# Kernel tuning notes

Hardware: AMD Instinct MI355X
Metric: run time of the kernel (lower is better)

The kernel has to match this reference:

```python
import jax, jax.numpy as jnp
import numpy as np

N = 100000      # num_nodes
E = 1600000     # num_edges (avg degree 16)
EMB = 128       # emb_dim
HID = 128       # hidden_size
REPR = 64       # repr_dim


def setup_inputs() -> dict:
    key = jax.random.key(0)
    k0, k1, k2, k3 = jax.random.split(key, 4)
    edge_index = jax.random.randint(k0, (2, E), 0, N)
    node_emb = jax.random.normal(k1, (N, EMB), jnp.float32) * 0.1
    # GCNConv weights: glorot-like init, bias zeros (PyG default)
    W1 = jax.random.normal(k2, (EMB, HID), jnp.float32) * (1.0 / np.sqrt(EMB))
    b1 = jnp.zeros((HID,), jnp.float32)
    W2 = jax.random.normal(k3, (HID, REPR), jnp.float32) * (1.0 / np.sqrt(HID))
    b2 = jnp.zeros((REPR,), jnp.float32)
    return {"edge_index": edge_index, "node_emb": node_emb,
            "W1": W1, "b1": b1, "W2": W2, "b2": b2}


def reference(edge_index, node_emb, W1, b1, W2, b2):
    # PyG GCNConv: add self-loops, symmetric degree normalization,
    # out = scatter_add(norm * (x W)[src] -> dst) + b
    loops = jnp.arange(N, dtype=edge_index.dtype)
    src = jnp.concatenate([edge_index[0], loops])  # [E+N]
    dst = jnp.concatenate([edge_index[1], loops])
    deg = jax.ops.segment_sum(jnp.ones_like(src, dtype=node_emb.dtype), dst,
                              num_segments=N)
    dinv = jax.lax.rsqrt(deg)  # deg >= 1 thanks to self-loops
    norm = dinv[src] * dinv[dst]  # [E+N]

    def gcn_conv(x, W, b):
        h = x @ W                                   # [N, out]
        msg = norm[:, None] * h[src]                # gather + scale, [E+N, out]
        return jax.ops.segment_sum(msg, dst, num_segments=N) + b

    x = jax.nn.relu(gcn_conv(node_emb, W1, b1))
    # F.dropout(training=False) is identity in eval mode
    return gcn_conv(x, W2, b2)
```

## Files before the change

### kernel.cpp

```cpp
#include <hip/hip_runtime.h>
#include <hip/hip_bf16.h>
#include <stdint.h>


static constexpr int KD = 128;
static constexpr int BSH = 9;
static constexpr int MAXB = 256;
static constexpr int CHUNK = 8192;
static constexpr int CAP = 12288;

typedef short bf16x8 __attribute__((ext_vector_type(8)));
typedef float f32x4  __attribute__((ext_vector_type(4)));
typedef float f32x2  __attribute__((ext_vector_type(2)));

__device__ __forceinline__ unsigned short f2bf(float f) {
    __hip_bfloat16 b = __float2bfloat16(f);
    return *reinterpret_cast<unsigned short*>(&b);
}
__device__ __forceinline__ float bflo(unsigned v) { return __uint_as_float(v << 16); }
__device__ __forceinline__ float bfhi(unsigned v) { return __uint_as_float(v & 0xffff0000u); }
__device__ __forceinline__ unsigned pk2(float lo, float hi) {
    return (unsigned)f2bf(lo) | ((unsigned)f2bf(hi) << 16);
}
__device__ __forceinline__ void accp(f32x2* a, uint4 v) {
    f32x2 t;
    t.x = bflo(v.x); t.y = bfhi(v.x); a[0] += t;
    t.x = bflo(v.y); t.y = bfhi(v.y); a[1] += t;
    t.x = bflo(v.z); t.y = bfhi(v.z); a[2] += t;
    t.x = bflo(v.w); t.y = bfhi(v.w); a[3] += t;
}

__global__ __launch_bounds__(256) void init_misc(const float* __restrict__ W1,
        const float* __restrict__ W2, unsigned short* __restrict__ Wt1,
        unsigned short* __restrict__ Wt2, int* __restrict__ bcur, int nbuck) {
    int t = blockIdx.x * 256 + threadIdx.x;
    if (t < 128 * 128) {
        int k = t >> 7, nn = t & 127;
        Wt1[nn * 128 + k] = f2bf(W1[t]);
    } else if (t < 128 * 128 + 128 * 64) {
        int i = t - 128 * 128;
        int k = i >> 6, nn = i & 63;
        Wt2[nn * 128 + k] = f2bf(W2[i]);
    } else if (t < 128 * 128 + 128 * 64 + MAXB) {
        int b = t - (128 * 128 + 128 * 64);
        bcur[b] = b * CAP;
    }
}

__global__ __launch_bounds__(256) void multisplit(const int* __restrict__ src,
        const int* __restrict__ dst, int* __restrict__ bcur,
        int* __restrict__ packed, int e, int nbuck) {
    __shared__ int cnt[MAXB], lbase[MAXB], wbase[MAXB], vcnt[MAXB], scanbuf[256];
    __shared__ int buf[CHUNK];
    const int t = threadIdx.x;
    const int e0 = blockIdx.x * CHUNK;
    const int m = min(CHUNK, e - e0);

    for (int i = t; i < nbuck; i += 256) cnt[i] = 0;
    __syncthreads();
    for (int i = t; i < m; i += 256) atomicAdd(&cnt[dst[e0 + i] >> BSH], 1);
    __syncthreads();
    int v = (t < nbuck) ? cnt[t] : 0;
    scanbuf[t] = v;
    __syncthreads();
    for (int off = 1; off < 256; off <<= 1) {
        int u = (t >= off) ? scanbuf[t - off] : 0;
        __syncthreads();
        scanbuf[t] += u;
        __syncthreads();
    }
    int excl = scanbuf[t] - v;
    if (t < nbuck) {
        lbase[t] = excl;
        vcnt[t] = v;
        wbase[t] = v ? atomicAdd(&bcur[t], v) : 0;
        cnt[t] = excl;
    }
    __syncthreads();
    for (int i = t; i < m; i += 256) {
        int d = dst[e0 + i], s = src[e0 + i];
        int b = d >> BSH;
        int p = atomicAdd(&cnt[b], 1);
        buf[p] = ((d & ((1 << BSH) - 1)) << 22) | s;
    }
    __syncthreads();
    int wv = t >> 6, ln = t & 63;
    for (int b = wv; b < nbuck; b += 4) {
        int c = vcnt[b], st = lbase[b], g = wbase[b];
        int end = min(c, (b + 1) * CAP - g);
        for (int i = ln; i < end; i += 64) packed[g + i] = buf[st + i];
    }
}

__global__ __launch_bounds__(256) void bucket_build(const int* __restrict__ packed,
        const int* __restrict__ bcur, int* __restrict__ roff, int* __restrict__ degN,
        float* __restrict__ dinv, int* __restrict__ csr, int n) {
    __shared__ int deg[1 << BSH];
    __shared__ int cur[1 << BSH];
    __shared__ int wsum[4];
    const int t = threadIdx.x;
    const int b = blockIdx.x;
    const int nodeBase = b << BSH;
    const int nn = min(1 << BSH, n - nodeBase);
    const int e0 = b * CAP, e1 = bcur[b];

    for (int i = t; i < (1 << BSH); i += 256) deg[i] = 0;
    __syncthreads();
    for (int i = e0 + t; i < e1; i += 256)
        atomicAdd(&deg[(unsigned)packed[i] >> 22], 1);
    __syncthreads();

    const int i0 = t * 2;
    int d0 = deg[i0], d1 = deg[i0 + 1];
    int tsum = d0 + d1;
    int lane = t & 63, wv = t >> 6;
    int v = tsum;
    for (int off = 1; off < 64; off <<= 1) {
        int u = __shfl_up(v, off, 64);
        if (lane >= off) v += u;
    }
    if (lane == 63) wsum[wv] = v;
    __syncthreads();
    int woff = 0;
    for (int i = 0; i < wv; ++i) woff += wsum[i];
    int excl = v - tsum + woff;
    int p0 = excl, p1 = excl + d0;
    cur[i0] = p0; cur[i0 + 1] = p1;
    if (i0 < nn) {
        roff[nodeBase + i0] = e0 + p0;
        degN[nodeBase + i0] = d0;
        dinv[nodeBase + i0] = rsqrtf((float)(d0 + 1));
    }
    if (i0 + 1 < nn) {
        roff[nodeBase + i0 + 1] = e0 + p1;
        degN[nodeBase + i0 + 1] = d1;
        dinv[nodeBase + i0 + 1] = rsqrtf((float)(d1 + 1));
    }
    __syncthreads();

    for (int i = e0 + t; i < e1; i += 256) {
        unsigned pk = (unsigned)packed[i];
        int dl = pk >> 22;
        int s = pk & 0x3FFFFF;
        int slot = atomicAdd(&cur[dl], 1);
        csr[e0 + slot] = s;
    }
}

template<int C, bool XBF>
__global__ __launch_bounds__(256) void gemm_mfma(const void* __restrict__ xv,
        const unsigned short* __restrict__ Wt, const float* __restrict__ dinv,
        unsigned short* __restrict__ out, int n)
{
    constexpr int KP = KD + 8;
    constexpr int WP = 64 + 8;
    __shared__ __align__(16) unsigned short xt[64 * KP];
    __shared__ __align__(16) unsigned short lw[C * WP];
    const int t = threadIdx.x;
    const int w = t >> 6, lane = t & 63;
    const int quad = lane >> 4, l16 = lane & 15;
    const int row0 = blockIdx.x * 64;

    for (int i = t; i < 64 * 32; i += 256) {
        int r = i >> 5, c4 = (i & 31) * 4;
        int row = row0 + r;
        ushort4 pk = make_ushort4(0, 0, 0, 0);
        if (row < n) {
            if constexpr (XBF) {
                pk = *reinterpret_cast<const ushort4*>(
                    &((const unsigned short*)xv)[(size_t)row * KD + c4]);
            } else {
                float4 v = *reinterpret_cast<const float4*>(
                    &((const float*)xv)[(size_t)row * KD + c4]);
                pk.x = f2bf(v.x); pk.y = f2bf(v.y); pk.z = f2bf(v.z); pk.w = f2bf(v.w);
            }
        }
        *reinterpret_cast<ushort4*>(&xt[r * KP + c4]) = pk;
    }

    f32x4 acc[C / 16];
#pragma unroll
    for (int i = 0; i < C / 16; ++i) acc[i] = (f32x4)(0.f);

    for (int h = 0; h < 2; ++h) {
        __syncthreads();
        for (int i = t; i < C * 16; i += 256) {
            int nr = i >> 4, j = (i & 15) * 4;
            *reinterpret_cast<ushort4*>(&lw[nr * WP + j]) =
                *reinterpret_cast<const ushort4*>(&Wt[nr * KD + h * 64 + j]);
        }
        __syncthreads();
#pragma unroll
        for (int kt = 0; kt < 2; ++kt) {
            bf16x8 af = *reinterpret_cast<const bf16x8*>(
                &xt[(w * 16 + l16) * KP + h * 64 + kt * 32 + quad * 8]);
#pragma unroll
            for (int ct = 0; ct < C / 16; ++ct) {
                bf16x8 bfr = *reinterpret_cast<const bf16x8*>(
                    &lw[(ct * 16 + l16) * WP + kt * 32 + quad * 8]);
                acc[ct] = __builtin_amdgcn_mfma_f32_16x16x32_bf16(af, bfr, acc[ct], 0, 0, 0);
            }
        }
    }

#pragma unroll
    for (int j = 0; j < 4; ++j) {
        int row = row0 + w * 16 + quad * 4 + j;
        if (row < n) {
            float s = dinv[row];
#pragma unroll
            for (int ct = 0; ct < C / 16; ++ct)
                out[(size_t)row * C + ct * 16 + l16] = f2bf(acc[ct][j] * s);
        }
    }
}

__global__ __launch_bounds__(256) void gather128(const uint4* __restrict__ H,
        const int* __restrict__ roff, const int* __restrict__ degN,
        const int* __restrict__ csr, const float* __restrict__ dinv,
        const float* __restrict__ b, uint4* __restrict__ out, int n)
{
    int wid = (blockIdx.x * 256 + threadIdx.x) >> 6;
    int lane = threadIdx.x & 63;
    if (wid >= n) return;
    const int qw = lane >> 4, cp = lane & 15;
    const char* Hb = (const char*)H;
    const unsigned cpo = (unsigned)cp * 16u;
    f32x2 a[4], c[4];
#pragma unroll
    for (int i = 0; i < 4; ++i) { a[i] = (f32x2)(0.f); c[i] = (f32x2)(0.f); }
    int e0 = roff[wid], e1 = e0 + degN[wid];
    for (int base = e0; base < e1; base += 64) {
        int m = e1 - base; if (m > 64) m = 64;
        int idx = (lane < m) ? csr[base + lane] : 0;
        int j = 0;
        for (; j + 8 <= m; j += 8) {
            unsigned u0 = (unsigned)__shfl(idx, j + qw);
            unsigned u1 = (unsigned)__shfl(idx, j + 4 + qw);
            uint4 v0 = *(const uint4*)(Hb + ((u0 << 8) + cpo));
            uint4 v1 = *(const uint4*)(Hb + ((u1 << 8) + cpo));
            accp(a, v0);
            accp(c, v1);
        }
        for (; j + 4 <= m; j += 4) {
            unsigned u = (unsigned)__shfl(idx, j + qw);
            uint4 v = *(const uint4*)(Hb + ((u << 8) + cpo));
            accp(a, v);
        }
        int r = m - j;
        if (r) {
            unsigned u = (unsigned)__shfl(idx, min(j + qw, m - 1));
            if (qw < r) {
                uint4 v = *(const uint4*)(Hb + ((u << 8) + cpo));
                accp(a, v);
            }
        }
    }
#pragma unroll
    for (int i = 0; i < 4; ++i) a[i] += c[i];
#pragma unroll
    for (int i = 0; i < 4; ++i) {
        a[i].x += __shfl_xor(a[i].x, 16, 64);
        a[i].x += __shfl_xor(a[i].x, 32, 64);
        a[i].y += __shfl_xor(a[i].y, 16, 64);
        a[i].y += __shfl_xor(a[i].y, 32, 64);
    }
    if (qw == 0) {
        uint4 sv = *(const uint4*)(Hb + (((unsigned)wid << 8) + cpo));
        accp(a, sv);
        float s = dinv[wid];
        float4 b0 = ((const float4*)b)[cp * 2];
        float4 b1 = ((const float4*)b)[cp * 2 + 1];
        float r0 = fmaxf(s * a[0].x + b0.x, 0.f), r1 = fmaxf(s * a[0].y + b0.y, 0.f);
        float r2 = fmaxf(s * a[1].x + b0.z, 0.f), r3 = fmaxf(s * a[1].y + b0.w, 0.f);
        float r4 = fmaxf(s * a[2].x + b1.x, 0.f), r5 = fmaxf(s * a[2].y + b1.y, 0.f);
        float r6 = fmaxf(s * a[3].x + b1.z, 0.f), r7 = fmaxf(s * a[3].y + b1.w, 0.f);
        uint4 o;
        o.x = pk2(r0, r1); o.y = pk2(r2, r3); o.z = pk2(r4, r5); o.w = pk2(r6, r7);
        out[(size_t)wid * 16 + cp] = o;
    }
}

__global__ __launch_bounds__(256) void gather64(const uint4* __restrict__ H,
        const int* __restrict__ roff, const int* __restrict__ degN,
        const int* __restrict__ csr, const float* __restrict__ dinv,
        const float* __restrict__ b, float4* __restrict__ out, int n)
{
    int wid = (blockIdx.x * 256 + threadIdx.x) >> 6;
    int lane = threadIdx.x & 63;
    if (wid >= n) return;
    const int oc = lane >> 3, cp = lane & 7;
    const char* Hb = (const char*)H;
    const unsigned cpo = (unsigned)cp * 16u;
    f32x2 a[4], c[4];
#pragma unroll
    for (int i = 0; i < 4; ++i) { a[i] = (f32x2)(0.f); c[i] = (f32x2)(0.f); }
    int e0 = roff[wid], e1 = e0 + degN[wid];
    for (int base = e0; base < e1; base += 64) {
        int m = e1 - base; if (m > 64) m = 64;
        int idx = (lane < m) ? csr[base + lane] : 0;
        int j = 0;
        for (; j + 16 <= m; j += 16) {
            unsigned u0 = (unsigned)__shfl(idx, j + oc);
            unsigned u1 = (unsigned)__shfl(idx, j + 8 + oc);
            uint4 v0 = *(const uint4*)(Hb + ((u0 << 7) + cpo));
            uint4 v1 = *(const uint4*)(Hb + ((u1 << 7) + cpo));
            accp(a, v0);
            accp(c, v1);
        }
        for (; j + 8 <= m; j += 8) {
            unsigned u = (unsigned)__shfl(idx, j + oc);
            uint4 v = *(const uint4*)(Hb + ((u << 7) + cpo));
            accp(a, v);
        }
        int r = m - j;
        if (r) {
            unsigned u = (unsigned)__shfl(idx, min(j + oc, m - 1));
            if (oc < r) {
                uint4 v = *(const uint4*)(Hb + ((u << 7) + cpo));
                accp(a, v);
            }
        }
    }
#pragma unroll
    for (int i = 0; i < 4; ++i) a[i] += c[i];
#pragma unroll
    for (int i = 0; i < 4; ++i) {
        a[i].x += __shfl_xor(a[i].x, 8, 64);
        a[i].x += __shfl_xor(a[i].x, 16, 64);
        a[i].x += __shfl_xor(a[i].x, 32, 64);
        a[i].y += __shfl_xor(a[i].y, 8, 64);
        a[i].y += __shfl_xor(a[i].y, 16, 64);
        a[i].y += __shfl_xor(a[i].y, 32, 64);
    }
    if (oc == 0) {
        uint4 sv = *(const uint4*)(Hb + (((unsigned)wid << 7) + cpo));
        accp(a, sv);
        float s = dinv[wid];
        float4 b0 = ((const float4*)b)[cp * 2];
        float4 b1 = ((const float4*)b)[cp * 2 + 1];
        float4 o0 = make_float4(s * a[0].x + b0.x, s * a[0].y + b0.y,
                                s * a[1].x + b0.z, s * a[1].y + b0.w);
        float4 o1 = make_float4(s * a[2].x + b1.x, s * a[2].y + b1.y,
                                s * a[3].x + b1.z, s * a[3].y + b1.w);
        out[(size_t)wid * 16 + cp * 2] = o0;
        out[(size_t)wid * 16 + cp * 2 + 1] = o1;
    }
}

extern "C" void kernel_launch(void* const* d_in, const int* in_sizes, int n_in,
                              void* d_out, int out_size, void* d_ws, size_t ws_size,
                              hipStream_t stream)
{
    const int* ei = (const int*)d_in[0];
    const int E = in_sizes[0] / 2;
    const float* emb = (const float*)d_in[1];
    const int N = in_sizes[1] / KD;
    const float* W1 = (const float*)d_in[2];
    const float* b1 = (const float*)d_in[3];
    const float* W2 = (const float*)d_in[4];
    const float* b2 = (const float*)d_in[5];
    const int* src = ei;
    const int* dst = ei + E;
    const int nbuck = (N + (1 << BSH) - 1) >> BSH;

    char* p = (char*)d_ws;
    auto alloc = [&](size_t bytes) { char* q = p; p += (bytes + 255) & ~(size_t)255; return q; };
    unsigned short* h1 = (unsigned short*)alloc((size_t)N * 128 * sizeof(unsigned short));
    unsigned short* x2 = (unsigned short*)alloc((size_t)N * 128 * sizeof(unsigned short));
    int*   csr    = (int*)  alloc((size_t)nbuck * CAP * sizeof(int));
    int*   packed = (int*)  alloc((size_t)nbuck * CAP * sizeof(int));
    int*   roff   = (int*)  alloc((size_t)N * sizeof(int));
    int*   degN   = (int*)  alloc((size_t)N * sizeof(int));
    float* dinv   = (float*)alloc((size_t)N * sizeof(float));
    int*   bcur   = (int*)  alloc(MAXB * sizeof(int));
    unsigned short* Wt1 = (unsigned short*)alloc(128 * 128 * sizeof(unsigned short));
    unsigned short* Wt2 = (unsigned short*)alloc(64 * 128 * sizeof(unsigned short));
    unsigned short* h2 = h1;

    init_misc<<<97, 256, 0, stream>>>(W1, W2, Wt1, Wt2, bcur, nbuck);
    multisplit<<<(E + CHUNK - 1) / CHUNK, 256, 0, stream>>>(src, dst, bcur, packed, E, nbuck);
    bucket_build<<<nbuck, 256, 0, stream>>>(packed, bcur, roff, degN, dinv, csr, N);

    gemm_mfma<128, false><<<(N + 63) / 64, 256, 0, stream>>>(emb, Wt1, dinv, h1, N);
    gather128<<<(N + 3) / 4, 256, 0, stream>>>((const uint4*)h1, roff, degN, csr,
                                               dinv, b1, (uint4*)x2, N);

    gemm_mfma<64, true><<<(N + 63) / 64, 256, 0, stream>>>(x2, Wt2, dinv, h2, N);
    gather64<<<(N + 3) / 4, 256, 0, stream>>>((const uint4*)h2, roff, degN, csr,
                                              dinv, b2, (float4*)d_out, N);
}
```

Measured before the change: 296.8 us.

## Count degrees with global atomics in multisplit, halve chunk, split gather128 launch

Per-node degree counting moves from a shared-memory atomic pass in bucket_build to global atomics inside multisplit, with init_misc now zeroing degN. The multisplit chunk size is halved, which doubles the block count and shrinks shared memory per block. The first-layer gather is also split into two launches over halves of the nodes. Global atomics on 1.6M random destinations add contention and memory traffic in exchange for dropping a re-read of the packed buffer, and the split launch adds launch overhead with no clear benefit.

```diff
diff --git a/kernel.cpp b/kernel.cpp
--- a/kernel.cpp
+++ b/kernel.cpp
@@ -6,7 +6,7 @@
 static constexpr int KD = 128;
 static constexpr int BSH = 9;
 static constexpr int MAXB = 256;
-static constexpr int CHUNK = 8192;
+static constexpr int CHUNK = 4096;
 static constexpr int CAP = 12288;
 
 typedef short bf16x8 __attribute__((ext_vector_type(8)));
@@ -32,7 +32,8 @@
 
 __global__ __launch_bounds__(256) void init_misc(const float* __restrict__ W1,
         const float* __restrict__ W2, unsigned short* __restrict__ Wt1,
-        unsigned short* __restrict__ Wt2, int* __restrict__ bcur, int nbuck) {
+        unsigned short* __restrict__ Wt2, int* __restrict__ bcur,
+        int* __restrict__ degN, int nbuck, int n) {
     int t = blockIdx.x * 256 + threadIdx.x;
     if (t < 128 * 128) {
         int k = t >> 7, nn = t & 127;
@@ -44,11 +45,14 @@
     } else if (t < 128 * 128 + 128 * 64 + MAXB) {
         int b = t - (128 * 128 + 128 * 64);
         bcur[b] = b * CAP;
+    } else {
+        int i = t - (128 * 128 + 128 * 64 + MAXB);
+        if (i < n) degN[i] = 0;
     }
 }
 
 __global__ __launch_bounds__(256) void multisplit(const int* __restrict__ src,
-        const int* __restrict__ dst, int* __restrict__ bcur,
+        const int* __restrict__ dst, int* __restrict__ bcur, int* __restrict__ degN,
         int* __restrict__ packed, int e, int nbuck) {
     __shared__ int cnt[MAXB], lbase[MAXB], wbase[MAXB], vcnt[MAXB], scanbuf[256];
     __shared__ int buf[CHUNK];
@@ -58,7 +62,11 @@
 
     for (int i = t; i < nbuck; i += 256) cnt[i] = 0;
     __syncthreads();
-    for (int i = t; i < m; i += 256) atomicAdd(&cnt[dst[e0 + i] >> BSH], 1);
+    for (int i = t; i < m; i += 256) {
+        int d = dst[e0 + i];
+        atomicAdd(&cnt[d >> BSH], 1);
+        atomicAdd(&degN[d], 1);
+    }
     __syncthreads();
     int v = (t < nbuck) ? cnt[t] : 0;
     scanbuf[t] = v;
@@ -93,9 +101,9 @@
 }
 
 __global__ __launch_bounds__(256) void bucket_build(const int* __restrict__ packed,
-        const int* __restrict__ bcur, int* __restrict__ roff, int* __restrict__ degN,
-        float* __restrict__ dinv, int* __restrict__ csr, int n) {
-    __shared__ int deg[1 << BSH];
+        const int* __restrict__ bcur, int* __restrict__ roff,
+        const int* __restrict__ degN, float* __restrict__ dinv,
+        int* __restrict__ csr, int n) {
     __shared__ int cur[1 << BSH];
     __shared__ int wsum[4];
     const int t = threadIdx.x;
@@ -104,14 +112,9 @@
     const int nn = min(1 << BSH, n - nodeBase);
     const int e0 = b * CAP, e1 = bcur[b];
 
-    for (int i = t; i < (1 << BSH); i += 256) deg[i] = 0;
-    __syncthreads();
-    for (int i = e0 + t; i < e1; i += 256)
-        atomicAdd(&deg[(unsigned)packed[i] >> 22], 1);
-    __syncthreads();
-
     const int i0 = t * 2;
-    int d0 = deg[i0], d1 = deg[i0 + 1];
+    int d0 = (i0     < nn) ? degN[nodeBase + i0]     : 0;
+    int d1 = (i0 + 1 < nn) ? degN[nodeBase + i0 + 1] : 0;
     int tsum = d0 + d1;
     int lane = t & 63, wv = t >> 6;
     int v = tsum;
@@ -128,12 +131,10 @@
     cur[i0] = p0; cur[i0 + 1] = p1;
     if (i0 < nn) {
         roff[nodeBase + i0] = e0 + p0;
-        degN[nodeBase + i0] = d0;
         dinv[nodeBase + i0] = rsqrtf((float)(d0 + 1));
     }
     if (i0 + 1 < nn) {
         roff[nodeBase + i0 + 1] = e0 + p1;
-        degN[nodeBase + i0 + 1] = d1;
         dinv[nodeBase + i0 + 1] = rsqrtf((float)(d1 + 1));
     }
     __syncthreads();
@@ -218,11 +219,11 @@
 __global__ __launch_bounds__(256) void gather128(const uint4* __restrict__ H,
         const int* __restrict__ roff, const int* __restrict__ degN,
         const int* __restrict__ csr, const float* __restrict__ dinv,
-        const float* __restrict__ b, uint4* __restrict__ out, int n)
+        const float* __restrict__ b, uint4* __restrict__ out, int n0, int n1)
 {
-    int wid = (blockIdx.x * 256 + threadIdx.x) >> 6;
+    int wid = n0 + ((blockIdx.x * 256 + threadIdx.x) >> 6);
     int lane = threadIdx.x & 63;
-    if (wid >= n) return;
+    if (wid >= n1) return;
     const int qw = lane >> 4, cp = lane & 15;
     const char* Hb = (const char*)H;
     const unsigned cpo = (unsigned)cp * 16u;
@@ -378,13 +379,19 @@
     unsigned short* Wt2 = (unsigned short*)alloc(64 * 128 * sizeof(unsigned short));
     unsigned short* h2 = h1;
 
-    init_misc<<<97, 256, 0, stream>>>(W1, W2, Wt1, Wt2, bcur, nbuck);
-    multisplit<<<(E + CHUNK - 1) / CHUNK, 256, 0, stream>>>(src, dst, bcur, packed, E, nbuck);
+    const int initThreads = 128 * 128 + 128 * 64 + MAXB + N;
+    init_misc<<<(initThreads + 255) / 256, 256, 0, stream>>>(W1, W2, Wt1, Wt2, bcur,
+                                                             degN, nbuck, N);
+    multisplit<<<(E + CHUNK - 1) / CHUNK, 256, 0, stream>>>(src, dst, bcur, degN,
+                                                            packed, E, nbuck);
     bucket_build<<<nbuck, 256, 0, stream>>>(packed, bcur, roff, degN, dinv, csr, N);
 
     gemm_mfma<128, false><<<(N + 63) / 64, 256, 0, stream>>>(emb, Wt1, dinv, h1, N);
-    gather128<<<(N + 3) / 4, 256, 0, stream>>>((const uint4*)h1, roff, degN, csr,
-                                               dinv, b1, (uint4*)x2, N);
+    const int half = ((N / 2) + 63) & ~63;
+    gather128<<<half / 4, 256, 0, stream>>>((const uint4*)h1, roff, degN, csr,
+                                            dinv, b1, (uint4*)x2, 0, half);
+    gather128<<<(N - half + 3) / 4, 256, 0, stream>>>((const uint4*)h1, roff, degN, csr,
+                                                      dinv, b1, (uint4*)x2, half, N);
 
     gemm_mfma<64, true><<<(N + 63) / 64, 256, 0, stream>>>(x2, Wt2, dinv, h2, N);
     gather64<<<(N + 3) / 4, 256, 0, stream>>>((const uint4*)h2, roff, degN, csr,
```

Result: slower. 348.0 us (+17.2%).
